# Optimization experiments

Hardware: AMD Instinct MI355X
Metric: run time of the kernel (lower is better)

The kernel has to match this reference:

```python
import jax, jax.numpy as jnp
import numpy as np

N_NODES = 10000
N_EDGES = 320000
D = 128  # feature dim for edges, nodes, globals


def setup_inputs() -> dict:
    key = jax.random.key(0)
    ks = jax.random.split(key, 8)
    edges = jax.random.normal(ks[0], (N_EDGES, D), dtype=jnp.float32)
    nodes = jax.random.normal(ks[1], (N_NODES, D), dtype=jnp.float32)
    globals_ = jax.random.normal(ks[2], (D,), dtype=jnp.float32)
    receivers = jax.random.randint(ks[3], (N_EDGES,), 0, N_NODES, dtype=jnp.int32).astype(jnp.int64)
    senders = jax.random.randint(ks[4], (N_EDGES,), 0, N_NODES, dtype=jnp.int32).astype(jnp.int64)
    W1 = jax.random.normal(ks[5], (4 * D, 256), dtype=jnp.float32) * (1.0 / np.sqrt(4 * D))
    b1 = jnp.zeros((256,), dtype=jnp.float32)
    W2 = jax.random.normal(ks[6], (256, D), dtype=jnp.float32) * (1.0 / np.sqrt(256))
    b2 = jnp.zeros((D,), dtype=jnp.float32)
    return {"edges": edges, "nodes": nodes, "globals_": globals_,
            "receivers": receivers, "senders": senders,
            "W1": W1, "b1": b1, "W2": W2, "b2": b2}


def reference(edges, nodes, globals_, receivers, senders, W1, b1, W2, b2):
    # Gather adjacent node features to edges, broadcast globals, concat.
    recv_feats = nodes[receivers]                 # [E, D]
    send_feats = nodes[senders]                   # [E, D]
    glob_feats = jnp.broadcast_to(globals_, (edges.shape[0], globals_.shape[0]))  # [E, D]
    x = jnp.concatenate([edges, recv_feats, send_feats, glob_feats], axis=-1)     # [E, 4D]
    # Edge-update MLP: 4D -> 256 -> D with relu.
    h = jax.nn.relu(x @ W1 + b1)
    new_edges = h @ W2 + b2                       # [E, D]
    return new_edges
```

## Files before the change

### kernel.cpp

```cpp
#include <hip/hip_runtime.h>
#include <hip/hip_bf16.h>

#define D 128
#define NH 256
#define BM 64
#define E_TOTAL 320000
#define NNODES 10000

typedef __attribute__((ext_vector_type(8))) short bf16x8;
typedef __attribute__((ext_vector_type(4))) float f32x4;

__device__ __forceinline__ unsigned short f2b(float f) {
  unsigned int u = __builtin_bit_cast(unsigned int, f);
  u += 0x7fffu + ((u >> 16) & 1u);
  return (unsigned short)(u >> 16);
}
__device__ __forceinline__ unsigned pk2(float a, float b) {
  return (unsigned)f2b(a) | ((unsigned)f2b(b) << 16);
}
__device__ __forceinline__ uint4 pack8(float4 a, float4 b) {
  uint4 r;
  r.x = pk2(a.x, a.y); r.y = pk2(a.z, a.w);
  r.z = pk2(b.x, b.y); r.w = pk2(b.z, b.w);
  return r;
}
__device__ __forceinline__ float lo2f(unsigned u) {
  return __builtin_bit_cast(float, u << 16);
}
__device__ __forceinline__ float hi2f(unsigned u) {
  return __builtin_bit_cast(float, u & 0xffff0000u);
}

__global__ void pack_w1_kernel(const float* __restrict__ W1,
                               ushort* __restrict__ W1pk) {
  int c = blockIdx.x * 256 + threadIdx.x;
  int s = c >> 12;
  int rem = c & 4095;
  int nt = rem >> 8;
  int rem2 = rem & 255;
  int ks = rem2 >> 6;
  int l = rem2 & 63;
  int col = nt * 16 + (l & 15);
  int k0 = s * 128 + ks * 32 + (l >> 4) * 8;
  ushort* dst = W1pk + (size_t)c * 8;
  #pragma unroll
  for (int j = 0; j < 8; ++j)
    dst[j] = f2b(W1[(size_t)(k0 + j) * NH + col]);
}

__global__ void pack_w2_kernel(const float* __restrict__ W2,
                               ushort* __restrict__ W2p) {
  int c = blockIdx.x * 256 + threadIdx.x;
  int nt2 = c / (8 * 64);
  int rem = c % (8 * 64);
  int ks = rem >> 6;
  int l = rem & 63;
  int col = nt2 * 16 + (l & 15);
  int k0 = ks * 32 + (l >> 4) * 8;
  ushort* dst = W2p + (size_t)c * 8;
  #pragma unroll
  for (int j = 0; j < 8; ++j)
    dst[j] = f2b(W2[(size_t)(k0 + j) * D + col]);
}

__global__ void cvec_kernel(const float* __restrict__ W1,
                            const float* __restrict__ b1,
                            const float* __restrict__ g,
                            float* __restrict__ cvec) {
  int n = threadIdx.x;
  float acc = b1[n];
  for (int k = 0; k < D; ++k)
    acc += g[k] * W1[(size_t)(384 + k) * NH + n];
  cvec[n] = acc;
}

__global__ __launch_bounds__(512, 4) void nodeh_kernel(
    const float* __restrict__ nodes,
    const ushort* __restrict__ W1pk,
    ushort* __restrict__ tblR,
    ushort* __restrict__ tblS) {
  __shared__ char Xn[BM * 256];
  const int role = blockIdx.y;
  ushort* __restrict__ tbl = role ? tblS : tblR;
  const int nb = blockIdx.x * BM;
  const int tid = threadIdx.x;

  {
    int row = tid >> 4;
    int cc = (tid & 15) * 16;
    #pragma unroll
    for (int q = 0; q < 2; ++q) {
      int r = row + q * 32;
      int rg = nb + r; if (rg >= NNODES) rg = NNODES - 1;
      const float* np = nodes + (size_t)rg * D + (tid & 15) * 8;
      float4 u0 = *(const float4*)np;
      float4 u1 = *(const float4*)(np + 4);
      *(uint4*)(Xn + r * 256 + (cc ^ ((r & 7) << 4))) = pack8(u0, u1);
    }
  }
  __syncthreads();

  const int lane = tid & 63;
  const int wave = tid >> 6;
  const int lr = lane & 15;
  const int kg = lane >> 4;

  const ushort* wb = W1pk + (size_t)(1 + role) * 32768
                   + (size_t)(wave * 2) * 2048 + lane * 8;
  f32x4 acc[2][4] = {};
  bf16x8 aw[2][2];
  #pragma unroll
  for (int ht = 0; ht < 2; ++ht)
    aw[0][ht] = *(const bf16x8*)(wb + ht * 2048);

  #pragma unroll
  for (int ks = 0; ks < 4; ++ks) {
    const int cur = ks & 1, nxt = cur ^ 1;
    if (ks < 3) {
      #pragma unroll
      for (int ht = 0; ht < 2; ++ht)
        aw[nxt][ht] = *(const bf16x8*)(wb + ht * 2048 + (ks + 1) * 512);
    }
    const int k0 = ks * 32 + kg * 8;
    bf16x8 xb[4];
    #pragma unroll
    for (int et = 0; et < 4; ++et) {
      int row = et * 16 + lr;
      xb[et] = *(const bf16x8*)(Xn + row * 256 + ((k0 * 2) ^ ((row & 7) << 4)));
    }
    #pragma unroll
    for (int ht = 0; ht < 2; ++ht)
      #pragma unroll
      for (int et = 0; et < 4; ++et)
        acc[ht][et] = __builtin_amdgcn_mfma_f32_16x16x32_bf16(aw[cur][ht], xb[et], acc[ht][et], 0, 0, 0);
  }

  #pragma unroll
  for (int ht = 0; ht < 2; ++ht) {
    int h0 = wave * 32 + ht * 16 + kg * 4;
    #pragma unroll
    for (int et = 0; et < 4; ++et) {
      int n = nb + et * 16 + lr;
      if (n < NNODES) {
        uint2 pk;
        pk.x = pk2(acc[ht][et][0], acc[ht][et][1]);
        pk.y = pk2(acc[ht][et][2], acc[ht][et][3]);
        *(uint2*)(tbl + (size_t)n * NH + h0) = pk;
      }
    }
  }
}

__global__ __launch_bounds__(512, 4) void fused_kernel(
    const float* __restrict__ edges,
    const int* __restrict__ receivers,
    const int* __restrict__ senders,
    const ushort* __restrict__ W1pk,
    const ushort* __restrict__ tblR,
    const ushort* __restrict__ tblS,
    const float* __restrict__ cvec,
    const ushort* __restrict__ W2p,
    const float* __restrict__ b2,
    float* __restrict__ out) {
  __shared__ char Xs[BM * 256];
  __shared__ char Hp[BM * 512];

  const int ebase = blockIdx.x * BM;
  const int tid = threadIdx.x;

  const int ge = tid >> 5;
  const int gc0 = (tid & 31) * 8;
  int idxR[4], idxS[4];
  #pragma unroll
  for (int j = 0; j < 4; ++j) {
    idxR[j] = receivers[ebase + ge + j * 16];
    idxS[j] = senders[ebase + ge + j * 16];
  }

  const int erow = tid >> 4;
  const int ecc = (tid & 15) * 16;
  float4 e0, e1, e2, e3;
  {
    const float* ep0 = edges + (size_t)(ebase + erow) * D + (tid & 15) * 8;
    e0 = *(const float4*)ep0;
    e1 = *(const float4*)(ep0 + 4);
    const float* ep1 = edges + (size_t)(ebase + erow + 32) * D + (tid & 15) * 8;
    e2 = *(const float4*)ep1;
    e3 = *(const float4*)(ep1 + 4);
  }

  float4 cva = *(const float4*)(cvec + gc0);
  float4 cvb = *(const float4*)(cvec + gc0 + 4);

  uint4 gR[4], gS[4];
  #pragma unroll
  for (int j = 0; j < 4; ++j) {
    gR[j] = *(const uint4*)(tblR + (size_t)idxR[j] * NH + gc0);
    gS[j] = *(const uint4*)(tblS + (size_t)idxS[j] * NH + gc0);
  }

  *(uint4*)(Xs + erow * 256 + (ecc ^ ((erow & 7) << 4))) = pack8(e0, e1);
  {
    int r2 = erow + 32;
    *(uint4*)(Xs + r2 * 256 + (ecc ^ ((r2 & 7) << 4))) = pack8(e2, e3);
  }

  #pragma unroll
  for (int j = 0; j < 4; ++j) {
    int e = ge + j * 16;
    float s0 = lo2f(gR[j].x) + lo2f(gS[j].x) + cva.x;
    float s1 = hi2f(gR[j].x) + hi2f(gS[j].x) + cva.y;
    float s2 = lo2f(gR[j].y) + lo2f(gS[j].y) + cva.z;
    float s3 = hi2f(gR[j].y) + hi2f(gS[j].y) + cva.w;
    float s4 = lo2f(gR[j].z) + lo2f(gS[j].z) + cvb.x;
    float s5 = hi2f(gR[j].z) + hi2f(gS[j].z) + cvb.y;
    float s6 = lo2f(gR[j].w) + lo2f(gS[j].w) + cvb.z;
    float s7 = hi2f(gR[j].w) + hi2f(gS[j].w) + cvb.w;
    uint4 o;
    o.x = pk2(s0, s1); o.y = pk2(s2, s3);
    o.z = pk2(s4, s5); o.w = pk2(s6, s7);
    *(uint4*)(Hp + e * 512 + ((gc0 * 2) ^ ((e & 7) << 4))) = o;
  }
  __syncthreads();

  const int lane = tid & 63;
  const int wave = tid >> 6;
  const int lr = lane & 15;
  const int kg = lane >> 4;
  const int wm3 = wave >> 1;
  const int wn3 = wave & 1;

  const ushort* w1base = W1pk + (size_t)(wave * 2) * 2048 + lane * 8;
  f32x4 acc[2][4] = {};
  bf16x8 aw[2][2];
  #pragma unroll
  for (int ht = 0; ht < 2; ++ht)
    aw[0][ht] = *(const bf16x8*)(w1base + ht * 2048);

  #pragma unroll
  for (int ks = 0; ks < 4; ++ks) {
    const int cur = ks & 1, nxt = cur ^ 1;
    if (ks < 3) {
      #pragma unroll
      for (int ht = 0; ht < 2; ++ht)
        aw[nxt][ht] = *(const bf16x8*)(w1base + ht * 2048 + (ks + 1) * 512);
    }
    const int k0 = ks * 32 + kg * 8;
    bf16x8 xb[4];
    #pragma unroll
    for (int et = 0; et < 4; ++et) {
      int row = et * 16 + lr;
      xb[et] = *(const bf16x8*)(Xs + row * 256 + ((k0 * 2) ^ ((row & 7) << 4)));
    }
    #pragma unroll
    for (int ht = 0; ht < 2; ++ht)
      #pragma unroll
      for (int et = 0; et < 4; ++et)
        acc[ht][et] = __builtin_amdgcn_mfma_f32_16x16x32_bf16(aw[cur][ht], xb[et], acc[ht][et], 0, 0, 0);
  }

  const ushort* w2base = W2p + (size_t)(wm3 * 2) * 8 * 512 + lane * 8;
  bf16x8 aw2[2][2];
  #pragma unroll
  for (int mt = 0; mt < 2; ++mt)
    aw2[0][mt] = *(const bf16x8*)(w2base + (size_t)mt * 8 * 512);

  #pragma unroll
  for (int ht = 0; ht < 2; ++ht) {
    const int h0b = (wave * 32 + ht * 16 + kg * 4) * 2;
    #pragma unroll
    for (int et = 0; et < 4; ++et) {
      int e = et * 16 + lr;
      char* p = Hp + e * 512 + (h0b ^ ((e & 7) << 4));
      uint2 hp = *(uint2*)p;
      float v0 = acc[ht][et][0] + lo2f(hp.x);
      float v1 = acc[ht][et][1] + hi2f(hp.x);
      float v2 = acc[ht][et][2] + lo2f(hp.y);
      float v3 = acc[ht][et][3] + hi2f(hp.y);
      v0 = v0 > 0.f ? v0 : 0.f;
      v1 = v1 > 0.f ? v1 : 0.f;
      v2 = v2 > 0.f ? v2 : 0.f;
      v3 = v3 > 0.f ? v3 : 0.f;
      uint2 pk;
      pk.x = pk2(v0, v1);
      pk.y = pk2(v2, v3);
      *(uint2*)p = pk;
    }
  }
  __syncthreads();

  float4 ba = *(const float4*)(b2 + wm3 * 32 + kg * 4);
  float4 bb2 = *(const float4*)(b2 + wm3 * 32 + 16 + kg * 4);
  f32x4 acc2[2][2] = {};
  #pragma unroll
  for (int ks = 0; ks < 8; ++ks) {
    const int cur = ks & 1, nxt = cur ^ 1;
    if (ks < 7) {
      #pragma unroll
      for (int mt = 0; mt < 2; ++mt)
        aw2[nxt][mt] = *(const bf16x8*)(w2base + (size_t)mt * 8 * 512 + (ks + 1) * 512);
    }
    const int k0 = ks * 32 + kg * 8;
    bf16x8 hb[2];
    #pragma unroll
    for (int et2 = 0; et2 < 2; ++et2) {
      int e = wn3 * 32 + et2 * 16 + lr;
      hb[et2] = *(const bf16x8*)(Hp + e * 512 + ((k0 * 2) ^ ((e & 7) << 4)));
    }
    #pragma unroll
    for (int mt = 0; mt < 2; ++mt)
      #pragma unroll
      for (int et2 = 0; et2 < 2; ++et2)
        acc2[mt][et2] = __builtin_amdgcn_mfma_f32_16x16x32_bf16(aw2[cur][mt], hb[et2], acc2[mt][et2], 0, 0, 0);
  }

  #pragma unroll
  for (int mt = 0; mt < 2; ++mt) {
    const float4 bq = mt ? bb2 : ba;
    const int c0 = wm3 * 32 + mt * 16 + kg * 4;
    #pragma unroll
    for (int et2 = 0; et2 < 2; ++et2) {
      int e = wn3 * 32 + et2 * 16 + lr;
      float4 o;
      o.x = acc2[mt][et2][0] + bq.x;
      o.y = acc2[mt][et2][1] + bq.y;
      o.z = acc2[mt][et2][2] + bq.z;
      o.w = acc2[mt][et2][3] + bq.w;
      *(float4*)(out + (size_t)(ebase + e) * D + c0) = o;
    }
  }
}

extern "C" void kernel_launch(void* const* d_in, const int* in_sizes, int n_in,
                              void* d_out, int out_size, void* d_ws, size_t ws_size,
                              hipStream_t stream) {
  const float* edges     = (const float*)d_in[0];
  const float* nodes     = (const float*)d_in[1];
  const float* globals_  = (const float*)d_in[2];
  const int*   receivers = (const int*)d_in[3];
  const int*   senders   = (const int*)d_in[4];
  const float* W1        = (const float*)d_in[5];
  const float* b1        = (const float*)d_in[6];
  const float* W2        = (const float*)d_in[7];
  const float* b2        = (const float*)d_in[8];
  float* out = (float*)d_out;

  char* ws = (char*)d_ws;
  ushort* W1pk = (ushort*)ws;
  ushort* W2p  = (ushort*)(ws + 196608);
  float*  cvec = (float*)(ws + 262144);
  ushort* tblR = (ushort*)(ws + 263168);
  ushort* tblS = (ushort*)(ws + 5383168);

  hipLaunchKernelGGL(pack_w1_kernel, dim3(48), dim3(256), 0, stream, W1, W1pk);
  hipLaunchKernelGGL(pack_w2_kernel, dim3(16), dim3(256), 0, stream, W2, W2p);
  hipLaunchKernelGGL(cvec_kernel, dim3(1), dim3(256), 0, stream,
                     W1, b1, globals_, cvec);
  hipLaunchKernelGGL(nodeh_kernel, dim3((NNODES + BM - 1) / BM, 2), dim3(512), 0, stream,
                     nodes, W1pk, tblR, tblS);
  hipLaunchKernelGGL(fused_kernel, dim3(E_TOTAL / BM), dim3(512), 0, stream,
                     edges, receivers, senders, W1pk, tblR, tblS, cvec, W2p, b2, out);
}
```

Before: 146.7 us.

## Gather node tables in MFMA layout, fold cvec into receiver table, merge prep kernels

```diff
diff --git a/kernel.cpp b/kernel.cpp
--- a/kernel.cpp
+++ b/kernel.cpp
@@ -31,52 +31,54 @@
   return __builtin_bit_cast(float, u & 0xffff0000u);
 }
 
-__global__ void pack_w1_kernel(const float* __restrict__ W1,
-                               ushort* __restrict__ W1pk) {
-  int c = blockIdx.x * 256 + threadIdx.x;
-  int s = c >> 12;
-  int rem = c & 4095;
-  int nt = rem >> 8;
-  int rem2 = rem & 255;
-  int ks = rem2 >> 6;
-  int l = rem2 & 63;
-  int col = nt * 16 + (l & 15);
-  int k0 = s * 128 + ks * 32 + (l >> 4) * 8;
-  ushort* dst = W1pk + (size_t)c * 8;
-  #pragma unroll
-  for (int j = 0; j < 8; ++j)
-    dst[j] = f2b(W1[(size_t)(k0 + j) * NH + col]);
-}
-
-__global__ void pack_w2_kernel(const float* __restrict__ W2,
-                               ushort* __restrict__ W2p) {
-  int c = blockIdx.x * 256 + threadIdx.x;
-  int nt2 = c / (8 * 64);
-  int rem = c % (8 * 64);
-  int ks = rem >> 6;
-  int l = rem & 63;
-  int col = nt2 * 16 + (l & 15);
-  int k0 = ks * 32 + (l >> 4) * 8;
-  ushort* dst = W2p + (size_t)c * 8;
-  #pragma unroll
-  for (int j = 0; j < 8; ++j)
-    dst[j] = f2b(W2[(size_t)(k0 + j) * D + col]);
-}
-
-__global__ void cvec_kernel(const float* __restrict__ W1,
+__global__ void prep_kernel(const float* __restrict__ W1,
+                            const float* __restrict__ W2,
                             const float* __restrict__ b1,
                             const float* __restrict__ g,
+                            ushort* __restrict__ W1pk,
+                            ushort* __restrict__ W2p,
                             float* __restrict__ cvec) {
-  int n = threadIdx.x;
-  float acc = b1[n];
-  for (int k = 0; k < D; ++k)
-    acc += g[k] * W1[(size_t)(384 + k) * NH + n];
-  cvec[n] = acc;
+  const int b = blockIdx.x;
+  const int tid = threadIdx.x;
+  if (b < 48) {
+    int c = b * 256 + tid;
+    int s = c >> 12;
+    int rem = c & 4095;
+    int nt = rem >> 8;
+    int rem2 = rem & 255;
+    int ks = rem2 >> 6;
+    int l = rem2 & 63;
+    int col = nt * 16 + (l & 15);
+    int k0 = s * 128 + ks * 32 + (l >> 4) * 8;
+    ushort* dst = W1pk + (size_t)c * 8;
+    #pragma unroll
+    for (int j = 0; j < 8; ++j)
+      dst[j] = f2b(W1[(size_t)(k0 + j) * NH + col]);
+  } else if (b < 64) {
+    int c = (b - 48) * 256 + tid;
+    int nt2 = c / (8 * 64);
+    int rem = c % (8 * 64);
+    int ks = rem >> 6;
+    int l = rem & 63;
+    int col = nt2 * 16 + (l & 15);
+    int k0 = ks * 32 + (l >> 4) * 8;
+    ushort* dst = W2p + (size_t)c * 8;
+    #pragma unroll
+    for (int j = 0; j < 8; ++j)
+      dst[j] = f2b(W2[(size_t)(k0 + j) * D + col]);
+  } else {
+    int n = tid;
+    float acc = b1[n];
+    for (int k = 0; k < D; ++k)
+      acc += g[k] * W1[(size_t)(384 + k) * NH + n];
+    cvec[n] = acc;
+  }
 }
 
 __global__ __launch_bounds__(512, 4) void nodeh_kernel(
     const float* __restrict__ nodes,
     const ushort* __restrict__ W1pk,
+    const float* __restrict__ cvec,
     ushort* __restrict__ tblR,
     ushort* __restrict__ tblS) {
   __shared__ char Xn[BM * 256];
@@ -138,13 +140,15 @@
   #pragma unroll
   for (int ht = 0; ht < 2; ++ht) {
     int h0 = wave * 32 + ht * 16 + kg * 4;
+    float4 cvq = {0.f, 0.f, 0.f, 0.f};
+    if (role == 0) cvq = *(const float4*)(cvec + h0);
     #pragma unroll
     for (int et = 0; et < 4; ++et) {
       int n = nb + et * 16 + lr;
       if (n < NNODES) {
         uint2 pk;
-        pk.x = pk2(acc[ht][et][0], acc[ht][et][1]);
-        pk.y = pk2(acc[ht][et][2], acc[ht][et][3]);
+        pk.x = pk2(acc[ht][et][0] + cvq.x, acc[ht][et][1] + cvq.y);
+        pk.y = pk2(acc[ht][et][2] + cvq.z, acc[ht][et][3] + cvq.w);
         *(uint2*)(tbl + (size_t)n * NH + h0) = pk;
       }
     }
@@ -158,7 +162,6 @@
     const ushort* __restrict__ W1pk,
     const ushort* __restrict__ tblR,
     const ushort* __restrict__ tblS,
-    const float* __restrict__ cvec,
     const ushort* __restrict__ W2p,
     const float* __restrict__ b2,
     float* __restrict__ out) {
@@ -167,84 +170,54 @@
 
   const int ebase = blockIdx.x * BM;
   const int tid = threadIdx.x;
-
-  const int ge = tid >> 5;
-  const int gc0 = (tid & 31) * 8;
-  int idxR[4], idxS[4];
-  #pragma unroll
-  for (int j = 0; j < 4; ++j) {
-    idxR[j] = receivers[ebase + ge + j * 16];
-    idxS[j] = senders[ebase + ge + j * 16];
-  }
-
-  const int erow = tid >> 4;
-  const int ecc = (tid & 15) * 16;
-  float4 e0, e1, e2, e3;
-  {
-    const float* ep0 = edges + (size_t)(ebase + erow) * D + (tid & 15) * 8;
-    e0 = *(const float4*)ep0;
-    e1 = *(const float4*)(ep0 + 4);
-    const float* ep1 = edges + (size_t)(ebase + erow + 32) * D + (tid & 15) * 8;
-    e2 = *(const float4*)ep1;
-    e3 = *(const float4*)(ep1 + 4);
-  }
-
-  float4 cva = *(const float4*)(cvec + gc0);
-  float4 cvb = *(const float4*)(cvec + gc0 + 4);
-
-  uint4 gR[4], gS[4];
-  #pragma unroll
-  for (int j = 0; j < 4; ++j) {
-    gR[j] = *(const uint4*)(tblR + (size_t)idxR[j] * NH + gc0);
-    gS[j] = *(const uint4*)(tblS + (size_t)idxS[j] * NH + gc0);
-  }
-
-  *(uint4*)(Xs + erow * 256 + (ecc ^ ((erow & 7) << 4))) = pack8(e0, e1);
-  {
-    int r2 = erow + 32;
-    *(uint4*)(Xs + r2 * 256 + (ecc ^ ((r2 & 7) << 4))) = pack8(e2, e3);
-  }
-
-  #pragma unroll
-  for (int j = 0; j < 4; ++j) {
-    int e = ge + j * 16;
-    float s0 = lo2f(gR[j].x) + lo2f(gS[j].x) + cva.x;
-    float s1 = hi2f(gR[j].x) + hi2f(gS[j].x) + cva.y;
-    float s2 = lo2f(gR[j].y) + lo2f(gS[j].y) + cva.z;
-    float s3 = hi2f(gR[j].y) + hi2f(gS[j].y) + cva.w;
-    float s4 = lo2f(gR[j].z) + lo2f(gS[j].z) + cvb.x;
-    float s5 = hi2f(gR[j].z) + hi2f(gS[j].z) + cvb.y;
-    float s6 = lo2f(gR[j].w) + lo2f(gS[j].w) + cvb.z;
-    float s7 = hi2f(gR[j].w) + hi2f(gS[j].w) + cvb.w;
-    uint4 o;
-    o.x = pk2(s0, s1); o.y = pk2(s2, s3);
-    o.z = pk2(s4, s5); o.w = pk2(s6, s7);
-    *(uint4*)(Hp + e * 512 + ((gc0 * 2) ^ ((e & 7) << 4))) = o;
-  }
-  __syncthreads();
-
   const int lane = tid & 63;
   const int wave = tid >> 6;
   const int lr = lane & 15;
   const int kg = lane >> 4;
-  const int wm3 = wave >> 1;
-  const int wn3 = wave & 1;
+
+  int idxR[4], idxS[4];
+  #pragma unroll
+  for (int et = 0; et < 4; ++et) {
+    idxR[et] = receivers[ebase + et * 16 + lr];
+    idxS[et] = senders[ebase + et * 16 + lr];
+  }
+
+  const int erow = tid >> 4;
+  const int ecc = (tid & 15) * 16;
+  {
+    const float* ep0 = edges + (size_t)(ebase + erow) * D + (tid & 15) * 8;
+    float4 e0 = *(const float4*)ep0;
+    float4 e1 = *(const float4*)(ep0 + 4);
+    const float* ep1 = edges + (size_t)(ebase + erow + 32) * D + (tid & 15) * 8;
+    float4 e2 = *(const float4*)ep1;
+    float4 e3 = *(const float4*)(ep1 + 4);
+    *(uint4*)(Xs + erow * 256 + (ecc ^ ((erow & 7) << 4))) = pack8(e0, e1);
+    int r2 = erow + 32;
+    *(uint4*)(Xs + r2 * 256 + (ecc ^ ((r2 & 7) << 4))) = pack8(e2, e3);
+  }
+  __syncthreads();
 
   const ushort* w1base = W1pk + (size_t)(wave * 2) * 2048 + lane * 8;
+  bf16x8 aw[4][2];
+  #pragma unroll
+  for (int ks = 0; ks < 4; ++ks)
+    #pragma unroll
+    for (int ht = 0; ht < 2; ++ht)
+      aw[ks][ht] = *(const bf16x8*)(w1base + ht * 2048 + ks * 512);
+
+  const int h0 = wave * 32 + kg * 4;
+  uint2 gR[2][4], gS[2][4];
+  #pragma unroll
+  for (int ht = 0; ht < 2; ++ht)
+    #pragma unroll
+    for (int et = 0; et < 4; ++et) {
+      gR[ht][et] = *(const uint2*)(tblR + (size_t)idxR[et] * NH + h0 + ht * 16);
+      gS[ht][et] = *(const uint2*)(tblS + (size_t)idxS[et] * NH + h0 + ht * 16);
+    }
+
   f32x4 acc[2][4] = {};
-  bf16x8 aw[2][2];
-  #pragma unroll
-  for (int ht = 0; ht < 2; ++ht)
-    aw[0][ht] = *(const bf16x8*)(w1base + ht * 2048);
-
   #pragma unroll
   for (int ks = 0; ks < 4; ++ks) {
-    const int cur = ks & 1, nxt = cur ^ 1;
-    if (ks < 3) {
-      #pragma unroll
-      for (int ht = 0; ht < 2; ++ht)
-        aw[nxt][ht] = *(const bf16x8*)(w1base + ht * 2048 + (ks + 1) * 512);
-    }
     const int k0 = ks * 32 + kg * 8;
     bf16x8 xb[4];
     #pragma unroll
@@ -256,27 +229,19 @@
     for (int ht = 0; ht < 2; ++ht)
       #pragma unroll
       for (int et = 0; et < 4; ++et)
-        acc[ht][et] = __builtin_amdgcn_mfma_f32_16x16x32_bf16(aw[cur][ht], xb[et], acc[ht][et], 0, 0, 0);
-  }
-
-  const ushort* w2base = W2p + (size_t)(wm3 * 2) * 8 * 512 + lane * 8;
-  bf16x8 aw2[2][2];
-  #pragma unroll
-  for (int mt = 0; mt < 2; ++mt)
-    aw2[0][mt] = *(const bf16x8*)(w2base + (size_t)mt * 8 * 512);
+        acc[ht][et] = __builtin_amdgcn_mfma_f32_16x16x32_bf16(aw[ks][ht], xb[et], acc[ht][et], 0, 0, 0);
+  }
 
   #pragma unroll
   for (int ht = 0; ht < 2; ++ht) {
-    const int h0b = (wave * 32 + ht * 16 + kg * 4) * 2;
+    const int h0b = (h0 + ht * 16) * 2;
     #pragma unroll
     for (int et = 0; et < 4; ++et) {
       int e = et * 16 + lr;
-      char* p = Hp + e * 512 + (h0b ^ ((e & 7) << 4));
-      uint2 hp = *(uint2*)p;
-      float v0 = acc[ht][et][0] + lo2f(hp.x);
-      float v1 = acc[ht][et][1] + hi2f(hp.x);
-      float v2 = acc[ht][et][2] + lo2f(hp.y);
-      float v3 = acc[ht][et][3] + hi2f(hp.y);
+      float v0 = acc[ht][et][0] + lo2f(gR[ht][et].x) + lo2f(gS[ht][et].x);
+      float v1 = acc[ht][et][1] + hi2f(gR[ht][et].x) + hi2f(gS[ht][et].x);
+      float v2 = acc[ht][et][2] + lo2f(gR[ht][et].y) + lo2f(gS[ht][et].y);
+      float v3 = acc[ht][et][3] + hi2f(gR[ht][et].y) + hi2f(gS[ht][et].y);
       v0 = v0 > 0.f ? v0 : 0.f;
       v1 = v1 > 0.f ? v1 : 0.f;
       v2 = v2 > 0.f ? v2 : 0.f;
@@ -284,9 +249,17 @@
       uint2 pk;
       pk.x = pk2(v0, v1);
       pk.y = pk2(v2, v3);
-      *(uint2*)p = pk;
-    }
-  }
+      *(uint2*)(Hp + e * 512 + (h0b ^ ((e & 7) << 4))) = pk;
+    }
+  }
+
+  const int wm3 = wave >> 1;
+  const int wn3 = wave & 1;
+  const ushort* w2base = W2p + (size_t)(wm3 * 2) * 8 * 512 + lane * 8;
+  bf16x8 aw2[2][2];
+  #pragma unroll
+  for (int mt = 0; mt < 2; ++mt)
+    aw2[0][mt] = *(const bf16x8*)(w2base + (size_t)mt * 8 * 512);
   __syncthreads();
 
   float4 ba = *(const float4*)(b2 + wm3 * 32 + kg * 4);
@@ -352,12 +325,10 @@
   ushort* tblR = (ushort*)(ws + 263168);
   ushort* tblS = (ushort*)(ws + 5383168);
 
-  hipLaunchKernelGGL(pack_w1_kernel, dim3(48), dim3(256), 0, stream, W1, W1pk);
-  hipLaunchKernelGGL(pack_w2_kernel, dim3(16), dim3(256), 0, stream, W2, W2p);
-  hipLaunchKernelGGL(cvec_kernel, dim3(1), dim3(256), 0, stream,
-                     W1, b1, globals_, cvec);
+  hipLaunchKernelGGL(prep_kernel, dim3(65), dim3(256), 0, stream,
+                     W1, W2, b1, globals_, W1pk, W2p, cvec);
   hipLaunchKernelGGL(nodeh_kernel, dim3((NNODES + BM - 1) / BM, 2), dim3(512), 0, stream,
-                     nodes, W1pk, tblR, tblS);
+                     nodes, W1pk, cvec, tblR, tblS);
   hipLaunchKernelGGL(fused_kernel, dim3(E_TOTAL / BM), dim3(512), 0, stream,
-                     edges, receivers, senders, W1pk, tblR, tblS, cvec, W2p, b2, out);
-}
+                     edges, receivers, senders, W1pk, tblR, tblS, W2p, b2, out);
+}
```

After: 187.3 us. +27.6%, slower.
